# Kernel optimization log

Hardware: AMD Instinct MI355X
Metric: run time of the kernel (lower is better)

Reference implementation:

```python
import jax, jax.numpy as jnp
import numpy as np

WS = 4          # window size per axis
HEADS = 3
HEAD_DIM = 32
DIM = 96
DISP = WS // 2  # displacement for shifted windows


def _make_mask(axis):
    # (w^3, w^3) additive mask, -inf across the wrap-around boundary on `axis`
    m = np.zeros((WS, WS, WS, WS, WS, WS), dtype=np.float32)
    d = DISP
    if axis == 0:
        m[-d:, :, :, :-d, :, :] = -np.inf
        m[:-d, :, :, -d:, :, :] = -np.inf
    elif axis == 1:
        m[:, -d:, :, :, :-d, :] = -np.inf
        m[:, :-d, :, :, -d:, :] = -np.inf
    else:
        m[:, :, -d:, :, :, :-d] = -np.inf
        m[:, :, :-d, :, :, -d:] = -np.inf
    return jnp.asarray(m.reshape(WS**3, WS**3))


def setup_inputs() -> dict:
    key = jax.random.key(0)
    k1, k2, k3, k4 = jax.random.split(key, 4)
    inner = HEADS * HEAD_DIM
    x = jax.random.normal(k1, (1, 64, 64, 64, DIM), dtype=jnp.float32)
    w_qkv = jax.random.normal(k2, (3 * inner, DIM), dtype=jnp.float32) * 0.02
    w_out = jax.random.normal(k3, (DIM, inner), dtype=jnp.float32) * 0.02
    b_out = jax.random.normal(k4, (DIM,), dtype=jnp.float32) * 0.02
    return {
        'x': x, 'w_qkv': w_qkv, 'w_out': w_out, 'b_out': b_out,
        'x_mask': _make_mask(0), 'y_mask': _make_mask(1), 'z_mask': _make_mask(2),
    }


def _forward(x, w_qkv, w_out, b_out, x_mask, y_mask, z_mask):
    scale = HEAD_DIM ** -0.5
    b, nx, ny, nz, _ = x.shape
    nwx, nwy, nwz = nx // WS, ny // WS, nz // WS
    seq = WS ** 3
    # cyclic shift by -displacement
    x = jnp.roll(x, shift=(-DISP, -DISP, -DISP), axis=(1, 2, 3))
    qkv = jnp.einsum('bxyzc,oc->bxyzo', x, w_qkv)
    q, k, v = jnp.split(qkv, 3, axis=-1)

    def win(t):  # -> (b, h, n_windows, seq, d)
        t = t.reshape(b, nwx, WS, nwy, WS, nwz, WS, HEADS, HEAD_DIM)
        t = t.transpose(0, 7, 1, 3, 5, 2, 4, 6, 8)
        return t.reshape(b, HEADS, nwx * nwy * nwz, seq, HEAD_DIM)

    q, k, v = win(q), win(k), win(v)
    dots = jnp.einsum('bhwid,bhwjd->bhwij', q, k) * scale

    # shifted-window masking (faithful to original einops relabeling, incl.
    # the final mislabeled rearrange which permutes the window grid)
    d = dots.reshape(b, HEADS, nwx, nwy, nwz, seq, seq)
    d = d.transpose(0, 1, 3, 4, 2, 5, 6)          # (b,h,ny,nz,nx,i,j)
    d = d.at[:, :, :, :, -1].add(x_mask)
    d = d.transpose(0, 1, 4, 3, 2, 5, 6)          # (b,h,nx,nz,ny,i,j)
    d = d.at[:, :, :, :, -1].add(y_mask)
    d = d.transpose(0, 1, 2, 4, 3, 5, 6)          # (b,h,nx,ny,nz,i,j)
    d = d.transpose(0, 1, 4, 2, 3, 5, 6)          # original's final rearrange bug
    dots = d.reshape(b, HEADS, nwx * nwy * nwz, seq, seq)

    attn = jax.nn.softmax(dots, axis=-1)
    out = jnp.einsum('bhwij,bhwjd->bhwid', attn, v)
    # un-window
    out = out.reshape(b, HEADS, nwx, nwy, nwz, WS, WS, WS, HEAD_DIM)
    out = out.transpose(0, 2, 5, 3, 6, 4, 7, 1, 8).reshape(b, nx, ny, nz, HEADS * HEAD_DIM)
    out = jnp.einsum('bxyzc,oc->bxyzo', out, w_out) + b_out
    # cyclic back shift
    return jnp.roll(out, shift=(DISP, DISP, DISP), axis=(1, 2, 3))


def reference(x, w_qkv, w_out, b_out, x_mask, y_mask, z_mask):
    return _forward(x, w_qkv, w_out, b_out, x_mask, y_mask, z_mask)
```

## Files before the change

kernel.cpp:

```cpp
#include <hip/hip_runtime.h>
#include <hip/hip_bf16.h>


using bf8   = __attribute__((ext_vector_type(8))) short;
using f32x4 = __attribute__((ext_vector_type(4))) float;

#define SQK 100
#define SP   68
#define SVT  68

__device__ __forceinline__ short f2b(float f) {
  __hip_bfloat16 h = __float2bfloat16(f);
  return *reinterpret_cast<short*>(&h);
}
__device__ __forceinline__ short4 pk4(const f32x4& a) {
  short4 s; s.x = f2b(a[0]); s.y = f2b(a[1]); s.z = f2b(a[2]); s.w = f2b(a[3]);
  return s;
}
__device__ __forceinline__ bf8 cvt8(const float4& a, const float4& b) {
  bf8 o;
  o[0] = f2b(a.x); o[1] = f2b(a.y); o[2] = f2b(a.z); o[3] = f2b(a.w);
  o[4] = f2b(b.x); o[5] = f2b(b.y); o[6] = f2b(b.z); o[7] = f2b(b.w);
  return o;
}

__global__ void prep_weights(const float* __restrict__ wq, const float* __restrict__ wo,
                             short* __restrict__ wqb, short* __restrict__ wob) {
  int i = blockIdx.x * 256 + threadIdx.x;
  const float QS = 0.17677669529663687f;
  if (i < 288 * 96) wqb[i] = f2b(wq[i] * (i < 96 * 96 ? QS : 1.0f));
  if (i < 96 * 96)  wob[i] = f2b(wo[i]);
}

__global__ __launch_bounds__(256, 4)
void fused_swin3d(const float* __restrict__ x,
                  const short* __restrict__ wqb,
                  const short* __restrict__ wob,
                  const float* __restrict__ bo,
                  float* __restrict__ out) {
  __shared__ __align__(16) short ls_q [64 * SQK];
  __shared__ __align__(16) short ls_k [64 * SQK];
  __shared__ __align__(16) short ls_vt[96 * SVT];

  const int w  = blockIdx.x;
  const int p  = w >> 8, q = (w >> 4) & 15, r = w & 15;
  const int tid  = threadIdx.x;
  const int lane = tid & 63;
  const int wv   = tid >> 6;
  const int lr   = lane & 15;
  const int kg   = lane >> 4;
  const int site = wv * 16 + lr;
  const int sy = (lr >> 2) & 3, sz = lr & 3;
  const int ch0 = kg * 8;

  const int gx1 = (q * 4 + wv + 2) & 63, gy1 = (r * 4 + sy + 2) & 63, gz1 = (p * 4 + sz + 2) & 63;
  const int gx2 = (p * 4 + wv + 2) & 63, gy2 = (q * 4 + sy + 2) & 63, gz2 = (r * 4 + sz + 2) & 63;
  const size_t b1 = (size_t)((gx1 * 64 + gy1) * 64 + gz1) * 96;
  const size_t b2 = (size_t)((gx2 * 64 + gy2) * 64 + gz2) * 96;

  float4 xa[6], xb[6];
  #pragma unroll
  for (int f = 0; f < 3; ++f) {
    xa[f]     = *reinterpret_cast<const float4*>(&x[b1 + f * 32 + ch0]);
    xa[3 + f] = *reinterpret_cast<const float4*>(&x[b1 + f * 32 + ch0 + 4]);
  }
  #pragma unroll
  for (int f = 0; f < 3; ++f) {
    xb[f]     = *reinterpret_cast<const float4*>(&x[b2 + f * 32 + ch0]);
    xb[3 + f] = *reinterpret_cast<const float4*>(&x[b2 + f * 32 + ch0 + 4]);
  }
  bf8 x1[3], x2[3];
  #pragma unroll
  for (int f = 0; f < 3; ++f) x1[f] = cvt8(xa[f], xa[3 + f]);

  #pragma unroll
  for (int n = 0; n < 12; ++n) {
    f32x4 acc = {0.f, 0.f, 0.f, 0.f};
    const short* wrow = &wqb[(n * 16 + lr) * 96 + ch0];
    acc = __builtin_amdgcn_mfma_f32_16x16x32_bf16(*reinterpret_cast<const bf8*>(wrow +  0), x1[0], acc, 0, 0, 0);
    acc = __builtin_amdgcn_mfma_f32_16x16x32_bf16(*reinterpret_cast<const bf8*>(wrow + 32), x1[1], acc, 0, 0, 0);
    acc = __builtin_amdgcn_mfma_f32_16x16x32_bf16(*reinterpret_cast<const bf8*>(wrow + 64), x1[2], acc, 0, 0, 0);
    short* dst = (n < 6) ? ls_q : ls_k;
    const int nn = (n < 6) ? n : n - 6;
    *reinterpret_cast<short4*>(&dst[site * SQK + nn * 16 + kg * 4]) = pk4(acc);
  }

  #pragma unroll
  for (int f = 0; f < 3; ++f) x2[f] = cvt8(xb[f], xb[3 + f]);
  #pragma unroll
  for (int n = 0; n < 6; ++n) {
    f32x4 acc = {0.f, 0.f, 0.f, 0.f};
    const short* wrow = &wqb[(192 + n * 16 + lr) * 96 + ch0];
    acc = __builtin_amdgcn_mfma_f32_16x16x32_bf16(x2[0], *reinterpret_cast<const bf8*>(wrow +  0), acc, 0, 0, 0);
    acc = __builtin_amdgcn_mfma_f32_16x16x32_bf16(x2[1], *reinterpret_cast<const bf8*>(wrow + 32), acc, 0, 0, 0);
    acc = __builtin_amdgcn_mfma_f32_16x16x32_bf16(x2[2], *reinterpret_cast<const bf8*>(wrow + 64), acc, 0, 0, 0);
    *reinterpret_cast<short4*>(&ls_vt[(n * 16 + lr) * SVT + wv * 16 + kg * 4]) = pk4(acc);
  }
  __syncthreads();

  const bf8 qa0 = *reinterpret_cast<const bf8*>(&ls_q[site * SQK +  0 + ch0]);
  const bf8 qa1 = *reinterpret_cast<const bf8*>(&ls_q[site * SQK + 32 + ch0]);
  const bf8 qa2 = *reinterpret_cast<const bf8*>(&ls_q[site * SQK + 64 + ch0]);

  const bool mx = (q == 15), my = (r == 15);
  const bool killy = my && ((lr >= 8) != (kg >= 2));
  const int  pbase = wv * 16 * SQK + lr * SP;

  f32x4 osw[3][2];
  #pragma unroll
  for (int h = 0; h < 3; ++h)
    #pragma unroll
    for (int n = 0; n < 2; ++n) osw[h][n] = (f32x4){0.f, 0.f, 0.f, 0.f};

  #pragma unroll
  for (int h = 0; h < 3; ++h) {
    const bf8 qa = (h == 0) ? qa0 : (h == 1) ? qa1 : qa2;
    f32x4 sv[4];
    #pragma unroll
    for (int n = 0; n < 4; ++n) {
      bf8 kb = *reinterpret_cast<const bf8*>(&ls_k[(n * 16 + lr) * SQK + h * 32 + ch0]);
      f32x4 z = {0.f, 0.f, 0.f, 0.f};
      sv[n] = __builtin_amdgcn_mfma_f32_16x16x32_bf16(kb, qa, z, 0, 0, 0);
    }
    float e[16];
    float sum = 0.f;
    #pragma unroll
    for (int n = 0; n < 4; ++n) {
      const bool kill = killy || (mx && ((wv >= 2) != (n >= 2)));
      #pragma unroll
      for (int t = 0; t < 4; ++t) {
        float ev = kill ? 0.f : __expf(sv[n][t]);
        e[n * 4 + t] = ev;
        sum += ev;
      }
    }
    sum += __shfl_xor(sum, 16);
    sum += __shfl_xor(sum, 32);
    const float inv = 1.f / sum;
    #pragma unroll
    for (int n = 0; n < 4; ++n) {
      f32x4 ep = { e[n * 4 + 0] * inv, e[n * 4 + 1] * inv,
                   e[n * 4 + 2] * inv, e[n * 4 + 3] * inv };
      *reinterpret_cast<short4*>(&ls_q[pbase + n * 16 + kg * 4]) = pk4(ep);
    }
    const bf8 pa0 = *reinterpret_cast<const bf8*>(&ls_q[pbase +  0 + ch0]);
    const bf8 pa1 = *reinterpret_cast<const bf8*>(&ls_q[pbase + 32 + ch0]);
    #pragma unroll
    for (int n = 0; n < 2; ++n) {
      bf8 vb0 = *reinterpret_cast<const bf8*>(&ls_vt[(h * 32 + n * 16 + lr) * SVT +  0 + ch0]);
      bf8 vb1 = *reinterpret_cast<const bf8*>(&ls_vt[(h * 32 + n * 16 + lr) * SVT + 32 + ch0]);
      osw[h][n] = __builtin_amdgcn_mfma_f32_16x16x32_bf16(vb0, pa0, osw[h][n], 0, 0, 0);
      osw[h][n] = __builtin_amdgcn_mfma_f32_16x16x32_bf16(vb1, pa1, osw[h][n], 0, 0, 0);
    }
  }

  #pragma unroll
  for (int h = 0; h < 3; ++h)
    #pragma unroll
    for (int n = 0; n < 2; ++n)
      *reinterpret_cast<short4*>(&ls_q[site * SQK + h * 32 + n * 16 + kg * 4]) = pk4(osw[h][n]);

  const bf8 oa0 = *reinterpret_cast<const bf8*>(&ls_q[site * SQK +  0 + ch0]);
  const bf8 oa1 = *reinterpret_cast<const bf8*>(&ls_q[site * SQK + 32 + ch0]);
  const bf8 oa2 = *reinterpret_cast<const bf8*>(&ls_q[site * SQK + 64 + ch0]);

  #pragma unroll
  for (int n = 0; n < 6; ++n) {
    f32x4 acc = {0.f, 0.f, 0.f, 0.f};
    const short* wrow = &wob[(n * 16 + lr) * 96 + ch0];
    acc = __builtin_amdgcn_mfma_f32_16x16x32_bf16(*reinterpret_cast<const bf8*>(wrow +  0), oa0, acc, 0, 0, 0);
    acc = __builtin_amdgcn_mfma_f32_16x16x32_bf16(*reinterpret_cast<const bf8*>(wrow + 32), oa1, acc, 0, 0, 0);
    acc = __builtin_amdgcn_mfma_f32_16x16x32_bf16(*reinterpret_cast<const bf8*>(wrow + 64), oa2, acc, 0, 0, 0);
    const float4 bb = *reinterpret_cast<const float4*>(&bo[n * 16 + kg * 4]);
    float4 o4;
    o4.x = acc[0] + bb.x; o4.y = acc[1] + bb.y;
    o4.z = acc[2] + bb.z; o4.w = acc[3] + bb.w;
    *reinterpret_cast<float4*>(&out[b2 + n * 16 + kg * 4]) = o4;
  }
}

extern "C" void kernel_launch(void* const* d_in, const int* in_sizes, int n_in,
                              void* d_out, int out_size, void* d_ws, size_t ws_size,
                              hipStream_t stream) {
  const float* x  = (const float*)d_in[0];
  const float* wq = (const float*)d_in[1];
  const float* wo = (const float*)d_in[2];
  const float* bo = (const float*)d_in[3];

  short* wqb = (short*)d_ws;
  short* wob = wqb + 288 * 96;

  prep_weights<<<(288 * 96 + 255) / 256, 256, 0, stream>>>(wq, wo, wqb, wob);
  fused_swin3d<<<4096, 256, 0, stream>>>(x, wqb, wob, bo, (float*)d_out);
}
```

Measured before the change: 109.2 us.

## Keep Q, P and attention output in registers via 16x16x16 MFMA layout

Drops the ls_q shared buffer by switching the attention and output-projection MFMAs to the 16x16x16 bf16 variant. With that variant the accumulator layout of one MFMA matches the B-operand layout of the next, so Q, the softmax probabilities and the attention output are passed straight from registers instead of round-tripping through LDS. The smaller LDS footprint lets launch bounds target 6 blocks per CU instead of 4. In exchange the kernel issues twice as many MFMAs at half the K depth, and the higher occupancy target may force register spills.

Result: slower. 127.9 us (+17.2%).

```diff
diff --git a/kernel.cpp b/kernel.cpp
--- a/kernel.cpp
+++ b/kernel.cpp
@@ -2,19 +2,24 @@
 #include <hip/hip_bf16.h>
 
 
+using bf4   = __attribute__((ext_vector_type(4))) short;
 using bf8   = __attribute__((ext_vector_type(8))) short;
 using f32x4 = __attribute__((ext_vector_type(4))) float;
 
 #define SQK 100
-#define SP   68
 #define SVT  68
 
 __device__ __forceinline__ short f2b(float f) {
   __hip_bfloat16 h = __float2bfloat16(f);
   return *reinterpret_cast<short*>(&h);
 }
-__device__ __forceinline__ short4 pk4(const f32x4& a) {
-  short4 s; s.x = f2b(a[0]); s.y = f2b(a[1]); s.z = f2b(a[2]); s.w = f2b(a[3]);
+__device__ __forceinline__ bf4 pk4(const f32x4& a) {
+  bf4 s; s[0] = f2b(a[0]); s[1] = f2b(a[1]); s[2] = f2b(a[2]); s[3] = f2b(a[3]);
+  return s;
+}
+__device__ __forceinline__ bf4 pk4s(const f32x4& a, float sc) {
+  bf4 s; s[0] = f2b(a[0] * sc); s[1] = f2b(a[1] * sc);
+  s[2] = f2b(a[2] * sc); s[3] = f2b(a[3] * sc);
   return s;
 }
 __device__ __forceinline__ bf8 cvt8(const float4& a, const float4& b) {
@@ -23,6 +28,21 @@
   o[4] = f2b(b.x); o[5] = f2b(b.y); o[6] = f2b(b.z); o[7] = f2b(b.w);
   return o;
 }
+
+#if __has_builtin(__builtin_amdgcn_mfma_f32_16x16x16bf16_1k)
+__device__ __forceinline__ f32x4 mfma16(bf4 a, bf4 b, f32x4 c) {
+  return __builtin_amdgcn_mfma_f32_16x16x16bf16_1k(a, b, c, 0, 0, 0);
+}
+#elif __has_builtin(__builtin_amdgcn_mfma_f32_16x16x16_bf16)
+__device__ __forceinline__ f32x4 mfma16(bf4 a, bf4 b, f32x4 c) {
+  return __builtin_amdgcn_mfma_f32_16x16x16_bf16(a, b, c, 0, 0, 0);
+}
+#else
+__device__ __forceinline__ f32x4 mfma16(bf4 a, bf4 b, f32x4 c) {
+  asm("v_mfma_f32_16x16x16_bf16 %0, %1, %2, %0" : "+v"(c) : "v"(a), "v"(b));
+  return c;
+}
+#endif
 
 __global__ void prep_weights(const float* __restrict__ wq, const float* __restrict__ wo,
                              short* __restrict__ wqb, short* __restrict__ wob) {
@@ -32,13 +52,12 @@
   if (i < 96 * 96)  wob[i] = f2b(wo[i]);
 }
 
-__global__ __launch_bounds__(256, 4)
+__global__ __launch_bounds__(256, 6)
 void fused_swin3d(const float* __restrict__ x,
                   const short* __restrict__ wqb,
                   const short* __restrict__ wob,
                   const float* __restrict__ bo,
                   float* __restrict__ out) {
-  __shared__ __align__(16) short ls_q [64 * SQK];
   __shared__ __align__(16) short ls_k [64 * SQK];
   __shared__ __align__(16) short ls_vt[96 * SVT];
 
@@ -69,10 +88,11 @@
     xb[f]     = *reinterpret_cast<const float4*>(&x[b2 + f * 32 + ch0]);
     xb[3 + f] = *reinterpret_cast<const float4*>(&x[b2 + f * 32 + ch0 + 4]);
   }
-  bf8 x1[3], x2[3];
+  bf8 x1[3];
   #pragma unroll
   for (int f = 0; f < 3; ++f) x1[f] = cvt8(xa[f], xa[3 + f]);
 
+  bf4 qn[6];
   #pragma unroll
   for (int n = 0; n < 12; ++n) {
     f32x4 acc = {0.f, 0.f, 0.f, 0.f};
@@ -80,11 +100,11 @@
     acc = __builtin_amdgcn_mfma_f32_16x16x32_bf16(*reinterpret_cast<const bf8*>(wrow +  0), x1[0], acc, 0, 0, 0);
     acc = __builtin_amdgcn_mfma_f32_16x16x32_bf16(*reinterpret_cast<const bf8*>(wrow + 32), x1[1], acc, 0, 0, 0);
     acc = __builtin_amdgcn_mfma_f32_16x16x32_bf16(*reinterpret_cast<const bf8*>(wrow + 64), x1[2], acc, 0, 0, 0);
-    short* dst = (n < 6) ? ls_q : ls_k;
-    const int nn = (n < 6) ? n : n - 6;
-    *reinterpret_cast<short4*>(&dst[site * SQK + nn * 16 + kg * 4]) = pk4(acc);
-  }
-
+    if (n < 6) qn[n] = pk4(acc);
+    else *reinterpret_cast<bf4*>(&ls_k[site * SQK + (n - 6) * 16 + kg * 4]) = pk4(acc);
+  }
+
+  bf8 x2[3];
   #pragma unroll
   for (int f = 0; f < 3; ++f) x2[f] = cvt8(xb[f], xb[3 + f]);
   #pragma unroll
@@ -94,17 +114,12 @@
     acc = __builtin_amdgcn_mfma_f32_16x16x32_bf16(x2[0], *reinterpret_cast<const bf8*>(wrow +  0), acc, 0, 0, 0);
     acc = __builtin_amdgcn_mfma_f32_16x16x32_bf16(x2[1], *reinterpret_cast<const bf8*>(wrow + 32), acc, 0, 0, 0);
     acc = __builtin_amdgcn_mfma_f32_16x16x32_bf16(x2[2], *reinterpret_cast<const bf8*>(wrow + 64), acc, 0, 0, 0);
-    *reinterpret_cast<short4*>(&ls_vt[(n * 16 + lr) * SVT + wv * 16 + kg * 4]) = pk4(acc);
+    *reinterpret_cast<bf4*>(&ls_vt[(n * 16 + lr) * SVT + wv * 16 + kg * 4]) = pk4(acc);
   }
   __syncthreads();
-
-  const bf8 qa0 = *reinterpret_cast<const bf8*>(&ls_q[site * SQK +  0 + ch0]);
-  const bf8 qa1 = *reinterpret_cast<const bf8*>(&ls_q[site * SQK + 32 + ch0]);
-  const bf8 qa2 = *reinterpret_cast<const bf8*>(&ls_q[site * SQK + 64 + ch0]);
 
   const bool mx = (q == 15), my = (r == 15);
   const bool killy = my && ((lr >= 8) != (kg >= 2));
-  const int  pbase = wv * 16 * SQK + lr * SP;
 
   f32x4 osw[3][2];
   #pragma unroll
@@ -114,68 +129,64 @@
 
   #pragma unroll
   for (int h = 0; h < 3; ++h) {
-    const bf8 qa = (h == 0) ? qa0 : (h == 1) ? qa1 : qa2;
     f32x4 sv[4];
     #pragma unroll
-    for (int n = 0; n < 4; ++n) {
-      bf8 kb = *reinterpret_cast<const bf8*>(&ls_k[(n * 16 + lr) * SQK + h * 32 + ch0]);
+    for (int nj = 0; nj < 4; ++nj) {
+      const int krow = (nj * 16 + lr) * SQK + h * 32 + kg * 4;
+      bf4 ka0 = *reinterpret_cast<const bf4*>(&ls_k[krow]);
+      bf4 ka1 = *reinterpret_cast<const bf4*>(&ls_k[krow + 16]);
       f32x4 z = {0.f, 0.f, 0.f, 0.f};
-      sv[n] = __builtin_amdgcn_mfma_f32_16x16x32_bf16(kb, qa, z, 0, 0, 0);
-    }
-    float e[16];
+      z = mfma16(ka0, qn[2 * h + 0], z);
+      sv[nj] = mfma16(ka1, qn[2 * h + 1], z);
+    }
     float sum = 0.f;
     #pragma unroll
-    for (int n = 0; n < 4; ++n) {
-      const bool kill = killy || (mx && ((wv >= 2) != (n >= 2)));
+    for (int nj = 0; nj < 4; ++nj) {
+      const bool kill = killy || (mx && ((wv >= 2) != (nj >= 2)));
       #pragma unroll
       for (int t = 0; t < 4; ++t) {
-        float ev = kill ? 0.f : __expf(sv[n][t]);
-        e[n * 4 + t] = ev;
+        float ev = kill ? 0.f : __expf(sv[nj][t]);
+        sv[nj][t] = ev;
         sum += ev;
       }
     }
     sum += __shfl_xor(sum, 16);
     sum += __shfl_xor(sum, 32);
     const float inv = 1.f / sum;
-    #pragma unroll
-    for (int n = 0; n < 4; ++n) {
-      f32x4 ep = { e[n * 4 + 0] * inv, e[n * 4 + 1] * inv,
-                   e[n * 4 + 2] * inv, e[n * 4 + 3] * inv };
-      *reinterpret_cast<short4*>(&ls_q[pbase + n * 16 + kg * 4]) = pk4(ep);
-    }
-    const bf8 pa0 = *reinterpret_cast<const bf8*>(&ls_q[pbase +  0 + ch0]);
-    const bf8 pa1 = *reinterpret_cast<const bf8*>(&ls_q[pbase + 32 + ch0]);
-    #pragma unroll
-    for (int n = 0; n < 2; ++n) {
-      bf8 vb0 = *reinterpret_cast<const bf8*>(&ls_vt[(h * 32 + n * 16 + lr) * SVT +  0 + ch0]);
-      bf8 vb1 = *reinterpret_cast<const bf8*>(&ls_vt[(h * 32 + n * 16 + lr) * SVT + 32 + ch0]);
-      osw[h][n] = __builtin_amdgcn_mfma_f32_16x16x32_bf16(vb0, pa0, osw[h][n], 0, 0, 0);
-      osw[h][n] = __builtin_amdgcn_mfma_f32_16x16x32_bf16(vb1, pa1, osw[h][n], 0, 0, 0);
-    }
-  }
-
+    bf4 pb[4];
+    #pragma unroll
+    for (int t = 0; t < 4; ++t) pb[t] = pk4s(sv[t], inv);
+    #pragma unroll
+    for (int nc = 0; nc < 2; ++nc) {
+      const int vrow = (h * 32 + nc * 16 + lr) * SVT + kg * 4;
+      #pragma unroll
+      for (int t = 0; t < 4; ++t) {
+        bf4 va = *reinterpret_cast<const bf4*>(&ls_vt[vrow + t * 16]);
+        osw[h][nc] = mfma16(va, pb[t], osw[h][nc]);
+      }
+    }
+  }
+
+  bf4 ob[6];
   #pragma unroll
   for (int h = 0; h < 3; ++h)
     #pragma unroll
-    for (int n = 0; n < 2; ++n)
-      *reinterpret_cast<short4*>(&ls_q[site * SQK + h * 32 + n * 16 + kg * 4]) = pk4(osw[h][n]);
-
-  const bf8 oa0 = *reinterpret_cast<const bf8*>(&ls_q[site * SQK +  0 + ch0]);
-  const bf8 oa1 = *reinterpret_cast<const bf8*>(&ls_q[site * SQK + 32 + ch0]);
-  const bf8 oa2 = *reinterpret_cast<const bf8*>(&ls_q[site * SQK + 64 + ch0]);
-
-  #pragma unroll
-  for (int n = 0; n < 6; ++n) {
+    for (int n = 0; n < 2; ++n) ob[2 * h + n] = pk4(osw[h][n]);
+
+  #pragma unroll
+  for (int no = 0; no < 6; ++no) {
     f32x4 acc = {0.f, 0.f, 0.f, 0.f};
-    const short* wrow = &wob[(n * 16 + lr) * 96 + ch0];
-    acc = __builtin_amdgcn_mfma_f32_16x16x32_bf16(*reinterpret_cast<const bf8*>(wrow +  0), oa0, acc, 0, 0, 0);
-    acc = __builtin_amdgcn_mfma_f32_16x16x32_bf16(*reinterpret_cast<const bf8*>(wrow + 32), oa1, acc, 0, 0, 0);
-    acc = __builtin_amdgcn_mfma_f32_16x16x32_bf16(*reinterpret_cast<const bf8*>(wrow + 64), oa2, acc, 0, 0, 0);
-    const float4 bb = *reinterpret_cast<const float4*>(&bo[n * 16 + kg * 4]);
+    const short* wr = &wob[(no * 16 + lr) * 96 + kg * 4];
+    #pragma unroll
+    for (int c = 0; c < 6; ++c) {
+      bf4 wa = *reinterpret_cast<const bf4*>(wr + c * 16);
+      acc = mfma16(wa, ob[c], acc);
+    }
+    const float4 bb = *reinterpret_cast<const float4*>(&bo[no * 16 + kg * 4]);
     float4 o4;
     o4.x = acc[0] + bb.x; o4.y = acc[1] + bb.y;
     o4.z = acc[2] + bb.z; o4.w = acc[3] + bb.w;
-    *reinterpret_cast<float4*>(&out[b2 + n * 16 + kg * 4]) = o4;
+    *reinterpret_cast<float4*>(&out[b2 + no * 16 + kg * 4]) = o4;
   }
 }
 
```
